# Performance work log

Measured on AMD Instinct MI355X. Metric: run time of the kernel, lower is better.

## Reference

```python
import jax, jax.numpy as jnp
import numpy as np

D_MODEL = 1024
N_HEADS = 16
D_HEAD = D_MODEL // N_HEADS


def setup_inputs() -> dict:
    key = jax.random.key(0)
    k1, k2, k3 = jax.random.split(key, 3)
    x = jax.random.normal(k1, (4, 2048, D_MODEL), dtype=jnp.float32)
    # torch Linear(d, 3d, bias=False): y = x @ W.T with W [3d, d].
    # We store the transposed form W_qkv [d, 3d] so y = x @ W_qkv (same math).
    scale = 1.0 / np.sqrt(D_MODEL)
    W_qkv = jax.random.normal(k2, (D_MODEL, 3 * D_MODEL), dtype=jnp.float32) * scale
    W_o = jax.random.normal(k3, (D_MODEL, D_MODEL), dtype=jnp.float32) * scale
    return {"x": x, "W_qkv": W_qkv, "W_o": W_o}


def reference(x, W_qkv, W_o):
    B, T, C = x.shape
    qkv = x @ W_qkv                              # [B, T, 3C]
    Q, K, V = jnp.split(qkv, 3, axis=-1)
    def to_heads(t):
        return t.reshape(B, T, N_HEADS, D_HEAD).transpose(0, 2, 1, 3)  # [B,H,T,d]
    Q, K, V = to_heads(Q), to_heads(K), to_heads(V)
    scores = jnp.einsum("bhqd,bhkd->bhqk", Q, K) / np.sqrt(D_HEAD)
    attn = jax.nn.softmax(scores, axis=-1)
    # dropout is identity in eval/deterministic mode
    context = jnp.einsum("bhqk,bhkd->bhqd", attn, V)
    context = context.transpose(0, 2, 1, 3).reshape(B, T, C)
    return context @ W_o
```

## Files before the change

kernel.cpp:

```cpp
#include <hip/hip_runtime.h>
#include <hip/hip_bf16.h>

typedef __attribute__((ext_vector_type(8))) short short8;
typedef __attribute__((ext_vector_type(4))) float f32x4;
typedef __attribute__((ext_vector_type(16))) float f32x16;
typedef __attribute__((ext_vector_type(2))) unsigned int uint2v;
typedef __attribute__((ext_vector_type(4))) unsigned int uint4v;

#define SEQ    2048
#define DM     1024
#define NH     16
#define DH     64
#define NBATCH 4
#define MTOK   (NBATCH * SEQ)
#define SEG    ((size_t)NBATCH * NH * SEQ * DH)
#define QSCALE 0.18033688f

static __device__ __forceinline__ unsigned bfbits(float f) {
  unsigned u = __float_as_uint(f);
  return u + 0x7fffu + ((u >> 16) & 1u);
}
static __device__ __forceinline__ unsigned short f2bf(float f) {
  return (unsigned short)(bfbits(f) >> 16);
}
static __device__ __forceinline__ unsigned pack2bf(float lo, float hi) {
  return __builtin_amdgcn_perm(bfbits(hi), bfbits(lo), 0x07060302u);
}
static __device__ __forceinline__ unsigned pack2tr(unsigned ulo, unsigned uhi) {
  return __builtin_amdgcn_perm(uhi, ulo, 0x07060302u);
}

typedef const __attribute__((address_space(1))) unsigned int* gp_t;
typedef __attribute__((address_space(3))) unsigned int* lp_t;
static __device__ __forceinline__ void gload_lds16(const void* g, void* l) {
  __builtin_amdgcn_global_load_lds((gp_t)g, (lp_t)l, 16, 0, 0);
}

template <bool WITH_X>
__global__ __launch_bounds__(256) void prep_kernel(
    const float* __restrict__ x, unsigned short* __restrict__ xb,
    const float* __restrict__ Wqkv, unsigned short* __restrict__ WqT,
    const float* __restrict__ Wo, unsigned short* __restrict__ WoT) {
  __shared__ float T[64][65];
  const int tid = threadIdx.x;
  int bid = blockIdx.x;
  if (WITH_X) {
    if (bid < 4096) {
      size_t i = ((size_t)bid * 256 + tid) * 8;
      f32x4 a = *(const f32x4*)&x[i];
      f32x4 b = *(const f32x4*)&x[i + 4];
      uint4v s;
      s[0] = pack2bf(a[0], a[1]);
      s[1] = pack2bf(a[2], a[3]);
      s[2] = pack2bf(b[0], b[1]);
      s[3] = pack2bf(b[2], b[3]);
      *(uint4v*)&xb[i] = s;
      return;
    }
    bid -= 4096;
  }
  const float* W;
  unsigned short* WT;
  int N, n0, k0;
  if (bid < 768) {
    W = Wqkv; WT = WqT; N = 3 * DM;
    n0 = (bid % 48) * 64; k0 = (bid / 48) * 64;
  } else {
    bid -= 768;
    W = Wo; WT = WoT; N = DM;
    n0 = (bid % 16) * 64; k0 = (bid / 16) * 64;
  }
#pragma unroll
  for (int it = 0; it < 4; it++) {
    int row = it * 16 + (tid >> 4);
    int c4 = (tid & 15) * 4;
    f32x4 v = *(const f32x4*)&W[(size_t)(k0 + row) * N + n0 + c4];
#pragma unroll
    for (int j = 0; j < 4; j++) T[row][c4 + j] = v[j];
  }
  __syncthreads();
#pragma unroll
  for (int it = 0; it < 2; it++) {
    int chunk = tid + it * 256;
    int n = chunk >> 3;
    int c8 = (chunk & 7) * 8;
    uint4v s;
#pragma unroll
    for (int j = 0; j < 4; j++)
      s[j] = pack2bf(T[c8 + 2 * j][n], T[c8 + 2 * j + 1][n]);
    *(uint4v*)&WT[(size_t)(n0 + n) * DM + k0 + c8] = s;
  }
}

__global__ __launch_bounds__(512, 2) void gemm256_qkv(
    const unsigned short* __restrict__ A, const unsigned short* __restrict__ BT,
    unsigned short* __restrict__ out0, unsigned short* __restrict__ out1,
    unsigned short* __restrict__ out2, int M, int N, int K) {
  __shared__ unsigned short As[2][256][64];
  __shared__ unsigned short Bs[2][256][64];

  const int tid = threadIdx.x;
  const int wave = tid >> 6;
  const int lane = tid & 63;
  const int quad = lane >> 4;
  const int lc = lane & 15;
  const int wr = wave >> 2;
  const int wc = wave & 3;
  const int m0 = blockIdx.y * 256;
  const int n0 = blockIdx.x * 256;
  const int xsw = lc & 7;
  const int lr8 = lane >> 3;
  const int sgo = ((lane & 7) ^ (lr8 & 7)) * 8;

  f32x4 acc[8][4];
#pragma unroll
  for (int i = 0; i < 8; i++)
#pragma unroll
    for (int j = 0; j < 4; j++) acc[i][j] = (f32x4){0.f, 0.f, 0.f, 0.f};

  const int NKT = K >> 6;

  auto stage = [&](int k0s, int buf) {
#pragma unroll
    for (int i = 0; i < 4; i++) {
      int rbase = i * 64 + wave * 8;
      gload_lds16(&A[(size_t)(m0 + rbase + lr8) * K + k0s + sgo],
                  &As[buf][rbase][0]);
      gload_lds16(&BT[(size_t)(n0 + rbase + lr8) * K + k0s + sgo],
                  &Bs[buf][rbase][0]);
    }
  };

  stage(0, 0);
  if (NKT > 1) stage(64, 1);
  asm volatile("s_waitcnt vmcnt(8)" ::: "memory");
  __builtin_amdgcn_sched_barrier(0);
  __builtin_amdgcn_s_barrier();
  __builtin_amdgcn_sched_barrier(0);

  for (int t = 0; t < NKT; t++) {
    const int cur = t & 1;
    short8 bB[4][2];
#pragma unroll
    for (int nt = 0; nt < 4; nt++)
#pragma unroll
      for (int kc = 0; kc < 2; kc++)
        bB[nt][kc] = *(const short8*)&Bs[cur][wc * 64 + nt * 16 + lc]
                                        [((kc * 4 + quad) ^ xsw) * 8];
#pragma unroll
    for (int mh = 0; mh < 2; mh++) {
      short8 aA[4][2];
#pragma unroll
      for (int m4 = 0; m4 < 4; m4++)
#pragma unroll
        for (int kc = 0; kc < 2; kc++)
          aA[m4][kc] = *(const short8*)&As[cur][wr * 128 + (mh * 4 + m4) * 16 + lc]
                                          [((kc * 4 + quad) ^ xsw) * 8];
      __builtin_amdgcn_s_setprio(1);
#pragma unroll
      for (int m4 = 0; m4 < 4; m4++)
#pragma unroll
        for (int nt = 0; nt < 4; nt++)
#pragma unroll
          for (int kc = 0; kc < 2; kc++)
            acc[mh * 4 + m4][nt] = __builtin_amdgcn_mfma_f32_16x16x32_bf16(
                aA[m4][kc], bB[nt][kc], acc[mh * 4 + m4][nt], 0, 0, 0);
      __builtin_amdgcn_s_setprio(0);
    }

    if (t + 1 < NKT) {
      asm volatile("s_waitcnt lgkmcnt(0)" ::: "memory");
      __builtin_amdgcn_sched_barrier(0);
      __builtin_amdgcn_s_barrier();
      __builtin_amdgcn_sched_barrier(0);
      if (t + 2 < NKT) {
        stage((t + 2) * 64, cur);
        asm volatile("s_waitcnt vmcnt(8)" ::: "memory");
      } else {
        asm volatile("s_waitcnt vmcnt(0)" ::: "memory");
      }
      __builtin_amdgcn_sched_barrier(0);
      __builtin_amdgcn_s_barrier();
      __builtin_amdgcn_sched_barrier(0);
    }
  }

  const int c = n0 >> 10;
#pragma unroll
  for (int mt = 0; mt < 8; mt++)
#pragma unroll
    for (int nt = 0; nt < 4; nt++) {
      int rb = m0 + wr * 128 + mt * 16 + quad * 4;
      int col = n0 + wc * 64 + nt * 16 + lc;
      int rem = col & 1023;
      int h = rem >> 6;
      int dd = rem & 63;
      int b = rb >> 11;
      int tt = rb & 2047;
      if (c == 2) {
        uint2v pk;
        pk[0] = pack2bf(acc[mt][nt][0], acc[mt][nt][1]);
        pk[1] = pack2bf(acc[mt][nt][2], acc[mt][nt][3]);
        *(uint2v*)&out2[(((size_t)(b * NH + h)) * DH + dd) * SEQ + tt] = pk;
      } else {
        unsigned short* dst = (c == 0) ? out0 : out1;
        float sc = (c == 0) ? QSCALE : 1.0f;
#pragma unroll
        for (int r = 0; r < 4; r++)
          dst[(((size_t)(b * NH + h) * SEQ + tt + r) << 6) + dd] =
              f2bf(acc[mt][nt][r] * sc);
      }
    }
}

template <int MODE>
__global__ __launch_bounds__(256) void gemm_kernel(
    const void* __restrict__ Av, const unsigned short* __restrict__ BT,
    unsigned short* __restrict__ out0, unsigned short* __restrict__ out1,
    unsigned short* __restrict__ out2, float* __restrict__ outf,
    int M, int N, int K) {
  __shared__ unsigned short As[128][64];
  __shared__ unsigned short Bs[128][64];

  const int tid = threadIdx.x;
  const int wave = tid >> 6;
  const int lane = tid & 63;
  const int quad = lane >> 4;
  const int lc = lane & 15;
  const int wr = wave >> 1;
  const int wc = wave & 1;
  const int m0 = blockIdx.y * 128;
  const int n0 = blockIdx.x * 128;
  const int xsw = lc & 7;
  const int lr8 = lane >> 3;
  const int sgo = ((lane & 7) ^ (lr8 & 7)) * 8;

  f32x4 acc[4][4];
#pragma unroll
  for (int i = 0; i < 4; i++)
#pragma unroll
    for (int j = 0; j < 4; j++) acc[i][j] = (f32x4){0.f, 0.f, 0.f, 0.f};

  for (int k0 = 0; k0 < K; k0 += 64) {
    if (MODE == 0) {
      const float* A = (const float*)Av;
#pragma unroll
      for (int i = 0; i < 4; i++) {
        int chunk = tid + i * 256;
        int r = chunk >> 3;
        int g = chunk & 7;
        int scol = (g ^ (r & 7)) * 8;
        f32x4 v0 = *(const f32x4*)&A[(size_t)(m0 + r) * K + k0 + scol];
        f32x4 v1 = *(const f32x4*)&A[(size_t)(m0 + r) * K + k0 + scol + 4];
        uint4v s;
        s[0] = pack2bf(v0[0], v0[1]);
        s[1] = pack2bf(v0[2], v0[3]);
        s[2] = pack2bf(v1[0], v1[1]);
        s[3] = pack2bf(v1[2], v1[3]);
        *(uint4v*)&As[r][g * 8] = s;
      }
    } else {
      const unsigned short* A = (const unsigned short*)Av;
#pragma unroll
      for (int it = 0; it < 4; it++) {
        int rbase = wave * 32 + it * 8;
        gload_lds16(&A[(size_t)(m0 + rbase + lr8) * K + k0 + sgo],
                    &As[rbase][0]);
      }
    }
#pragma unroll
    for (int it = 0; it < 4; it++) {
      int rbase = wave * 32 + it * 8;
      gload_lds16(&BT[(size_t)(n0 + rbase + lr8) * K + k0 + sgo],
                  &Bs[rbase][0]);
    }
    __syncthreads();

#pragma unroll
    for (int kc = 0; kc < 2; kc++) {
      short8 aA[4], bB[4];
#pragma unroll
      for (int mt = 0; mt < 4; mt++)
        aA[mt] = *(const short8*)&As[wr * 64 + mt * 16 + lc]
                                    [((kc * 4 + quad) ^ xsw) * 8];
#pragma unroll
      for (int nt = 0; nt < 4; nt++)
        bB[nt] = *(const short8*)&Bs[wc * 64 + nt * 16 + lc]
                                    [((kc * 4 + quad) ^ xsw) * 8];
#pragma unroll
      for (int mt = 0; mt < 4; mt++)
#pragma unroll
        for (int nt = 0; nt < 4; nt++)
          acc[mt][nt] = __builtin_amdgcn_mfma_f32_16x16x32_bf16(
              aA[mt], bB[nt], acc[mt][nt], 0, 0, 0);
    }
    __syncthreads();
  }

  const int c = n0 >> 10;
#pragma unroll
  for (int mt = 0; mt < 4; mt++)
#pragma unroll
    for (int nt = 0; nt < 4; nt++) {
      int rb = m0 + wr * 64 + mt * 16 + quad * 4;
      int col = n0 + wc * 64 + nt * 16 + lc;
      if (MODE == 1) {
#pragma unroll
        for (int r = 0; r < 4; r++)
          outf[(size_t)(rb + r) * N + col] = acc[mt][nt][r];
      } else {
        int rem = col & 1023;
        int h = rem >> 6;
        int dd = rem & 63;
        int b = rb >> 11;
        int tt = rb & 2047;
        if (c == 2) {
          uint2v pk;
          pk[0] = pack2bf(acc[mt][nt][0], acc[mt][nt][1]);
          pk[1] = pack2bf(acc[mt][nt][2], acc[mt][nt][3]);
          *(uint2v*)&out2[(((size_t)(b * NH + h)) * DH + dd) * SEQ + tt] = pk;
        } else {
          unsigned short* dst = (c == 0) ? out0 : out1;
          float sc = (c == 0) ? QSCALE : 1.0f;
#pragma unroll
          for (int r = 0; r < 4; r++)
            dst[(((size_t)(b * NH + h) * SEQ + tt + r) << 6) + dd] =
                f2bf(acc[mt][nt][r] * sc);
        }
      }
    }
}

__global__ __launch_bounds__(256, 4) void attn_kernel(
    const unsigned short* __restrict__ Q, const unsigned short* __restrict__ K,
    const unsigned short* __restrict__ Vt, unsigned short* __restrict__ ctx) {
  __shared__ unsigned short KsL[2][64 * 64];
  __shared__ unsigned short VtL[2][64 * 64];

  const int tid = threadIdx.x;
  const int wave = tid >> 6;
  const int lane = tid & 63;
  const int half = lane >> 5;
  const int l31 = lane & 31;
  const int id = blockIdx.x;
  const int bh = (id & 7) * 8 + (id >> 3) / 16;
  const int qt = (id >> 3) & 15;
  const int q0 = qt * 128 + wave * 32;
  const unsigned kqbase = (unsigned)bh * (SEQ * DH);
  const unsigned vbase = (unsigned)bh * (DH * SEQ);

  short8 bQ[4];
#pragma unroll
  for (int dc = 0; dc < 4; dc++)
    bQ[dc] = *(const short8*)&Q[kqbase + (unsigned)(q0 + l31) * DH + dc * 16 + half * 8];

  f32x16 o[2], o_l;
#pragma unroll
  for (int nb = 0; nb < 2; nb++)
#pragma unroll
    for (int j = 0; j < 16; j++) o[nb][j] = 0.f;
#pragma unroll
  for (int j = 0; j < 16; j++) o_l[j] = 0.f;

  union { unsigned u[4]; short8 s8; } onesu;
#pragma unroll
  for (int j = 0; j < 4; j++) onesu.u[j] = 0x3f803f80u;
  const short8 ones = onesu.s8;

  const int xsw = l31 & 7;
  const int g0 = wave * 128 + lane;
  const int r0 = g0 >> 3;
  const unsigned sgo = ((g0 & 7) ^ (r0 & 7)) * 8;
  const unsigned so0 = (unsigned)r0 * DH + sgo;
  const unsigned sv0 = (unsigned)r0 * SEQ + sgo;
  const int ldo = wave * 1024;

  auto stage = [&](int kt, int b) {
    const unsigned kg = kqbase + (unsigned)kt * (64 * DH);
    const unsigned vg = vbase + (unsigned)kt * 64;
    unsigned short* kd = &KsL[b][ldo];
    unsigned short* vd = &VtL[b][ldo];
    gload_lds16(&K[kg + so0], kd);
    gload_lds16(&K[kg + so0 + 8 * DH], kd + 512);
    gload_lds16(&Vt[vg + sv0], vd);
    gload_lds16(&Vt[vg + sv0 + 8 * SEQ], vd + 512);
  };

  stage(0, 0);
  __syncthreads();

  for (int kt = 0; kt < SEQ / 64; kt++) {
    const int cur = kt & 1;
    if (kt + 1 < SEQ / 64) stage(kt + 1, cur ^ 1);
    const unsigned short* kcur = &KsL[cur][0];
    const unsigned short* vcur = &VtL[cur][0];

#pragma unroll
    for (int kb = 0; kb < 2; kb++) {
      f32x16 s;
#pragma unroll
      for (int j = 0; j < 16; j++) s[j] = 0.f;
      __builtin_amdgcn_s_setprio(1);
#pragma unroll
      for (int dc = 0; dc < 4; dc++) {
        const short8 aK = *(const short8*)&kcur[(unsigned)(kb * 32 + l31) * 64 +
                                                ((dc * 2 + half) ^ xsw) * 8];
        s = __builtin_amdgcn_mfma_f32_32x32x16_bf16(aK, bQ[dc], s, 0, 0, 0);
      }
      __builtin_amdgcn_s_setprio(0);

      unsigned d0[4], d1[4];
#pragma unroll
      for (int gq = 0; gq < 4; gq++) {
        unsigned u0 = __float_as_uint(__builtin_amdgcn_exp2f(s[gq * 4 + 0]));
        unsigned u1 = __float_as_uint(__builtin_amdgcn_exp2f(s[gq * 4 + 1]));
        unsigned u2 = __float_as_uint(__builtin_amdgcn_exp2f(s[gq * 4 + 2]));
        unsigned u3 = __float_as_uint(__builtin_amdgcn_exp2f(s[gq * 4 + 3]));
        d0[gq] = pack2tr(u0, u1);
        d1[gq] = pack2tr(u2, u3);
      }

#pragma unroll
      for (int kcl = 0; kcl < 2; kcl++) {
        unsigned w0 = d0[kcl * 2], w2 = d0[kcl * 2 + 1];
        unsigned w1 = d1[kcl * 2], w3 = d1[kcl * 2 + 1];
        asm("v_permlane32_swap_b32 %0, %1" : "+v"(w0), "+v"(w2));
        asm("v_permlane32_swap_b32 %0, %1" : "+v"(w1), "+v"(w3));
        union { unsigned u[4]; short8 s8; } cv;
        cv.u[0] = w0; cv.u[1] = w1; cv.u[2] = w2; cv.u[3] = w3;
        const int kc = kb * 2 + kcl;
        __builtin_amdgcn_s_setprio(1);
#pragma unroll
        for (int nb = 0; nb < 2; nb++) {
          const short8 bV = *(const short8*)&vcur[(unsigned)(nb * 32 + l31) * 64 +
                                                  ((kc * 2 + half) ^ xsw) * 8];
          o[nb] = __builtin_amdgcn_mfma_f32_32x32x16_bf16(cv.s8, bV, o[nb], 0, 0, 0);
        }
        o_l = __builtin_amdgcn_mfma_f32_32x32x16_bf16(cv.s8, ones, o_l, 0, 0, 0);
        __builtin_amdgcn_s_setprio(0);
      }
    }
    __syncthreads();
  }

  const int b = bh >> 4;
  const int h = bh & 15;
#pragma unroll
  for (int gq = 0; gq < 4; gq++)
#pragma unroll
    for (int j = 0; j < 4; j++) {
      int r = gq * 4 + j;
      int ql = j + gq * 8 + half * 4;
      float inv = __builtin_amdgcn_rcpf(o_l[r]);
      int token = qt * 128 + wave * 32 + ql;
#pragma unroll
      for (int nb = 0; nb < 2; nb++)
        ctx[((size_t)b * SEQ + token) * DM + h * DH + nb * 32 + l31] =
            f2bf(o[nb][r] * inv);
    }
}

extern "C" void kernel_launch(void* const* d_in, const int* in_sizes, int n_in,
                              void* d_out, int out_size, void* d_ws,
                              size_t ws_size, hipStream_t stream) {
  const float* x = (const float*)d_in[0];
  const float* Wqkv = (const float*)d_in[1];
  const float* Wo = (const float*)d_in[2];
  float* out = (float*)d_out;
  unsigned short* ws = (unsigned short*)d_ws;

  unsigned short* Qb = ws;
  unsigned short* Kb = ws + SEG;
  unsigned short* Vt = ws + 2 * SEG;
  unsigned short* Ctx = ws + 3 * SEG;
  unsigned short* WqT = Ctx + (size_t)MTOK * DM;
  unsigned short* WoT = WqT + (size_t)3 * DM * DM;
  unsigned short* Xb = WoT + (size_t)DM * DM;
  const size_t need =
      ((size_t)(Xb - ws) + (size_t)MTOK * DM) * sizeof(unsigned short);

  if (ws_size >= need) {
    prep_kernel<true><<<dim3(4096 + 768 + 256), 256, 0, stream>>>(
        x, Xb, Wqkv, WqT, Wo, WoT);
    gemm256_qkv<<<dim3(3 * DM / 256, MTOK / 256), 512, 0, stream>>>(
        Xb, WqT, Qb, Kb, Vt, MTOK, 3 * DM, DM);
  } else {
    prep_kernel<false><<<dim3(768 + 256), 256, 0, stream>>>(
        x, nullptr, Wqkv, WqT, Wo, WoT);
    gemm_kernel<0><<<dim3(3 * DM / 128, MTOK / 128), 256, 0, stream>>>(
        (const void*)x, WqT, Qb, Kb, Vt, nullptr, MTOK, 3 * DM, DM);
  }
  attn_kernel<<<dim3(SEQ / 128 * NBATCH * NH), 256, 0, stream>>>(Qb, Kb, Vt, Ctx);
  gemm_kernel<1><<<dim3(DM / 128, MTOK / 128), 256, 0, stream>>>(
      (const void*)Ctx, WoT, nullptr, nullptr, nullptr, out, MTOK, DM, DM);
}
```

Measured before the change: 280.2 us.

## Interleave QKV GEMM prefetch with MFMA halves, remap blocks per XCD, shrink out-proj tile

The 256x256 QKV GEMM now issues the next-tile global-to-LDS loads in pieces between its two MFMA halves instead of as one batch after all compute. This requires reusing the current buffer's A rows only after they have been read, which the extra barriers enforce. Both GEMMs switch to a 1D grid whose block ids are remapped so that each of the 8 XCD groups gets a contiguous range of M tiles, aimed at L2 locality. The output projection uses 128x64 tiles with launch_bounds occupancy 4 so more blocks run concurrently, at the cost of more A-tile reloads.

```diff
diff --git a/kernel.cpp b/kernel.cpp
--- a/kernel.cpp
+++ b/kernel.cpp
@@ -106,11 +106,16 @@
   const int lc = lane & 15;
   const int wr = wave >> 2;
   const int wc = wave & 3;
-  const int m0 = blockIdx.y * 256;
-  const int n0 = blockIdx.x * 256;
+  const int id = blockIdx.x;
+  const int nxb = N >> 8;
+  const int mbx = (M >> 8) >> 3;
+  const int idx = id >> 3;
+  const int m0 = ((id & 7) * mbx + idx / nxb) * 256;
+  const int n0 = (idx % nxb) * 256;
   const int xsw = lc & 7;
   const int lr8 = lane >> 3;
-  const int sgo = ((lane & 7) ^ (lr8 & 7)) * 8;
+  const int sgo = ((lane & 7) ^ lr8) * 8;
+  const int NKT = K >> 6;
 
   f32x4 acc[8][4];
 #pragma unroll
@@ -118,21 +123,21 @@
 #pragma unroll
     for (int j = 0; j < 4; j++) acc[i][j] = (f32x4){0.f, 0.f, 0.f, 0.f};
 
-  const int NKT = K >> 6;
-
-  auto stage = [&](int k0s, int buf) {
-#pragma unroll
-    for (int i = 0; i < 4; i++) {
-      int rbase = i * 64 + wave * 8;
-      gload_lds16(&A[(size_t)(m0 + rbase + lr8) * K + k0s + sgo],
-                  &As[buf][rbase][0]);
-      gload_lds16(&BT[(size_t)(n0 + rbase + lr8) * K + k0s + sgo],
-                  &Bs[buf][rbase][0]);
-    }
+  auto stageA = [&](int k0s, int buf, int u) {
+    int r = u * 64 + wave * 8;
+    gload_lds16(&A[(size_t)(m0 + r + lr8) * K + k0s + sgo], &As[buf][r][0]);
   };
-
-  stage(0, 0);
-  if (NKT > 1) stage(64, 1);
+  auto stageB = [&](int k0s, int buf, int u) {
+    int r = u * 64 + wave * 8;
+    gload_lds16(&BT[(size_t)(n0 + r + lr8) * K + k0s + sgo], &Bs[buf][r][0]);
+  };
+  auto stage_all = [&](int k0s, int buf) {
+#pragma unroll
+    for (int u = 0; u < 4; u++) { stageA(k0s, buf, u); stageB(k0s, buf, u); }
+  };
+
+  stage_all(0, 0);
+  if (NKT > 1) stage_all(64, 1);
   asm volatile("s_waitcnt vmcnt(8)" ::: "memory");
   __builtin_amdgcn_sched_barrier(0);
   __builtin_amdgcn_s_barrier();
@@ -140,6 +145,9 @@
 
   for (int t = 0; t < NKT; t++) {
     const int cur = t & 1;
+    const bool pre = (t + 2 < NKT);
+    const int kpre = (t + 2) * 64;
+
     short8 bB[4][2];
 #pragma unroll
     for (int nt = 0; nt < 4; nt++)
@@ -147,42 +155,65 @@
       for (int kc = 0; kc < 2; kc++)
         bB[nt][kc] = *(const short8*)&Bs[cur][wc * 64 + nt * 16 + lc]
                                         [((kc * 4 + quad) ^ xsw) * 8];
-#pragma unroll
-    for (int mh = 0; mh < 2; mh++) {
-      short8 aA[4][2];
-#pragma unroll
-      for (int m4 = 0; m4 < 4; m4++)
+    short8 aA[4][2];
+#pragma unroll
+    for (int m4 = 0; m4 < 4; m4++)
+#pragma unroll
+      for (int kc = 0; kc < 2; kc++)
+        aA[m4][kc] = *(const short8*)&As[cur][wr * 128 + m4 * 16 + lc]
+                                        [((kc * 4 + quad) ^ xsw) * 8];
+    __builtin_amdgcn_s_setprio(1);
+#pragma unroll
+    for (int m4 = 0; m4 < 4; m4++)
+#pragma unroll
+      for (int nt = 0; nt < 4; nt++)
 #pragma unroll
         for (int kc = 0; kc < 2; kc++)
-          aA[m4][kc] = *(const short8*)&As[cur][wr * 128 + (mh * 4 + m4) * 16 + lc]
-                                          [((kc * 4 + quad) ^ xsw) * 8];
-      __builtin_amdgcn_s_setprio(1);
-#pragma unroll
-      for (int m4 = 0; m4 < 4; m4++)
-#pragma unroll
-        for (int nt = 0; nt < 4; nt++)
-#pragma unroll
-          for (int kc = 0; kc < 2; kc++)
-            acc[mh * 4 + m4][nt] = __builtin_amdgcn_mfma_f32_16x16x32_bf16(
-                aA[m4][kc], bB[nt][kc], acc[mh * 4 + m4][nt], 0, 0, 0);
-      __builtin_amdgcn_s_setprio(0);
-    }
-
-    if (t + 1 < NKT) {
-      asm volatile("s_waitcnt lgkmcnt(0)" ::: "memory");
-      __builtin_amdgcn_sched_barrier(0);
-      __builtin_amdgcn_s_barrier();
-      __builtin_amdgcn_sched_barrier(0);
-      if (t + 2 < NKT) {
-        stage((t + 2) * 64, cur);
-        asm volatile("s_waitcnt vmcnt(8)" ::: "memory");
-      } else {
-        asm volatile("s_waitcnt vmcnt(0)" ::: "memory");
-      }
-      __builtin_amdgcn_sched_barrier(0);
-      __builtin_amdgcn_s_barrier();
-      __builtin_amdgcn_sched_barrier(0);
-    }
+          acc[m4][nt] = __builtin_amdgcn_mfma_f32_16x16x32_bf16(
+              aA[m4][kc], bB[nt][kc], acc[m4][nt], 0, 0, 0);
+    __builtin_amdgcn_s_setprio(0);
+    asm volatile("s_waitcnt lgkmcnt(0)" ::: "memory");
+    __builtin_amdgcn_sched_barrier(0);
+    __builtin_amdgcn_s_barrier();
+    __builtin_amdgcn_sched_barrier(0);
+
+    if (pre) {
+      stageA(kpre, cur, 0);
+      stageA(kpre, cur, 2);
+      stageB(kpre, cur, 0); stageB(kpre, cur, 1);
+      stageB(kpre, cur, 2); stageB(kpre, cur, 3);
+    }
+#pragma unroll
+    for (int m4 = 0; m4 < 4; m4++)
+#pragma unroll
+      for (int kc = 0; kc < 2; kc++)
+        aA[m4][kc] = *(const short8*)&As[cur][wr * 128 + 64 + m4 * 16 + lc]
+                                        [((kc * 4 + quad) ^ xsw) * 8];
+    __builtin_amdgcn_s_setprio(1);
+#pragma unroll
+    for (int m4 = 0; m4 < 4; m4++)
+#pragma unroll
+      for (int nt = 0; nt < 4; nt++)
+#pragma unroll
+        for (int kc = 0; kc < 2; kc++)
+          acc[4 + m4][nt] = __builtin_amdgcn_mfma_f32_16x16x32_bf16(
+              aA[m4][kc], bB[nt][kc], acc[4 + m4][nt], 0, 0, 0);
+    __builtin_amdgcn_s_setprio(0);
+    asm volatile("s_waitcnt lgkmcnt(0)" ::: "memory");
+    __builtin_amdgcn_sched_barrier(0);
+    __builtin_amdgcn_s_barrier();
+    __builtin_amdgcn_sched_barrier(0);
+
+    if (pre) {
+      stageA(kpre, cur, 1);
+      stageA(kpre, cur, 3);
+      asm volatile("s_waitcnt vmcnt(8)" ::: "memory");
+    } else {
+      asm volatile("s_waitcnt vmcnt(0)" ::: "memory");
+    }
+    __builtin_amdgcn_sched_barrier(0);
+    __builtin_amdgcn_s_barrier();
+    __builtin_amdgcn_sched_barrier(0);
   }
 
   const int c = n0 >> 10;
@@ -213,31 +244,36 @@
     }
 }
 
-template <int MODE>
-__global__ __launch_bounds__(256) void gemm_kernel(
+template <int MODE, int TN>
+__global__ __launch_bounds__(256, 4) void gemm_kernel(
     const void* __restrict__ Av, const unsigned short* __restrict__ BT,
     unsigned short* __restrict__ out0, unsigned short* __restrict__ out1,
     unsigned short* __restrict__ out2, float* __restrict__ outf,
     int M, int N, int K) {
+  constexpr int MT = (TN == 128) ? 4 : 2;
   __shared__ unsigned short As[128][64];
-  __shared__ unsigned short Bs[128][64];
+  __shared__ unsigned short Bs[TN][64];
 
   const int tid = threadIdx.x;
   const int wave = tid >> 6;
   const int lane = tid & 63;
   const int quad = lane >> 4;
   const int lc = lane & 15;
-  const int wr = wave >> 1;
-  const int wc = wave & 1;
-  const int m0 = blockIdx.y * 128;
-  const int n0 = blockIdx.x * 128;
+  const int wr = (TN == 128) ? (wave >> 1) : wave;
+  const int wc = (TN == 128) ? (wave & 1) : 0;
+  const int id = blockIdx.x;
+  const int nxb = N / TN;
+  const int mbx = (M >> 7) >> 3;
+  const int idx = id >> 3;
+  const int m0 = ((id & 7) * mbx + idx / nxb) * 128;
+  const int n0 = (idx % nxb) * TN;
   const int xsw = lc & 7;
   const int lr8 = lane >> 3;
   const int sgo = ((lane & 7) ^ (lr8 & 7)) * 8;
 
-  f32x4 acc[4][4];
-#pragma unroll
-  for (int i = 0; i < 4; i++)
+  f32x4 acc[MT][4];
+#pragma unroll
+  for (int i = 0; i < MT; i++)
 #pragma unroll
     for (int j = 0; j < 4; j++) acc[i][j] = (f32x4){0.f, 0.f, 0.f, 0.f};
 
@@ -269,8 +305,8 @@
       }
     }
 #pragma unroll
-    for (int it = 0; it < 4; it++) {
-      int rbase = wave * 32 + it * 8;
+    for (int it = 0; it < TN / 32; it++) {
+      int rbase = wave * (TN / 4) + it * 8;
       gload_lds16(&BT[(size_t)(n0 + rbase + lr8) * K + k0 + sgo],
                   &Bs[rbase][0]);
     }
@@ -278,17 +314,17 @@
 
 #pragma unroll
     for (int kc = 0; kc < 2; kc++) {
-      short8 aA[4], bB[4];
-#pragma unroll
-      for (int mt = 0; mt < 4; mt++)
-        aA[mt] = *(const short8*)&As[wr * 64 + mt * 16 + lc]
+      short8 aA[MT], bB[4];
+#pragma unroll
+      for (int mt = 0; mt < MT; mt++)
+        aA[mt] = *(const short8*)&As[wr * (MT * 16) + mt * 16 + lc]
                                     [((kc * 4 + quad) ^ xsw) * 8];
 #pragma unroll
       for (int nt = 0; nt < 4; nt++)
         bB[nt] = *(const short8*)&Bs[wc * 64 + nt * 16 + lc]
                                     [((kc * 4 + quad) ^ xsw) * 8];
 #pragma unroll
-      for (int mt = 0; mt < 4; mt++)
+      for (int mt = 0; mt < MT; mt++)
 #pragma unroll
         for (int nt = 0; nt < 4; nt++)
           acc[mt][nt] = __builtin_amdgcn_mfma_f32_16x16x32_bf16(
@@ -299,10 +335,10 @@
 
   const int c = n0 >> 10;
 #pragma unroll
-  for (int mt = 0; mt < 4; mt++)
+  for (int mt = 0; mt < MT; mt++)
 #pragma unroll
     for (int nt = 0; nt < 4; nt++) {
-      int rb = m0 + wr * 64 + mt * 16 + quad * 4;
+      int rb = m0 + wr * (MT * 16) + mt * 16 + quad * 4;
       int col = n0 + wc * 64 + nt * 16 + lc;
       if (MODE == 1) {
 #pragma unroll
@@ -482,15 +518,15 @@
   if (ws_size >= need) {
     prep_kernel<true><<<dim3(4096 + 768 + 256), 256, 0, stream>>>(
         x, Xb, Wqkv, WqT, Wo, WoT);
-    gemm256_qkv<<<dim3(3 * DM / 256, MTOK / 256), 512, 0, stream>>>(
+    gemm256_qkv<<<dim3((3 * DM / 256) * (MTOK / 256)), 512, 0, stream>>>(
         Xb, WqT, Qb, Kb, Vt, MTOK, 3 * DM, DM);
   } else {
     prep_kernel<false><<<dim3(768 + 256), 256, 0, stream>>>(
         x, nullptr, Wqkv, WqT, Wo, WoT);
-    gemm_kernel<0><<<dim3(3 * DM / 128, MTOK / 128), 256, 0, stream>>>(
+    gemm_kernel<0, 128><<<dim3((3 * DM / 128) * (MTOK / 128)), 256, 0, stream>>>(
         (const void*)x, WqT, Qb, Kb, Vt, nullptr, MTOK, 3 * DM, DM);
   }
   attn_kernel<<<dim3(SEQ / 128 * NBATCH * NH), 256, 0, stream>>>(Qb, Kb, Vt, Ctx);
-  gemm_kernel<1><<<dim3(DM / 128, MTOK / 128), 256, 0, stream>>>(
+  gemm_kernel<1, 64><<<dim3((DM / 64) * (MTOK / 128)), 256, 0, stream>>>(
       (const void*)Ctx, WoT, nullptr, nullptr, nullptr, out, MTOK, DM, DM);
 }
```

Result: no change. 280.0 us (-0.1%).
